# Performance work log

Measured on AMD Instinct MI355X. Metric: run time of the kernel, lower is better.

## Reference

```python
import jax, jax.numpy as jnp
import numpy as np

B, T, D, H = 4096, 200, 128, 128


def setup_inputs() -> dict:
    key = jax.random.key(0)
    ks = jax.random.split(key, 9)
    s = 1.0 / np.sqrt(D + H)  # torch Linear default init bound
    u = lambda k, shape: jax.random.uniform(k, shape, jnp.float32, -s, s)
    return {
        "inputs": jax.random.normal(ks[0], (B, T, D), jnp.float32),
        "attention_scores": jax.random.uniform(ks[1], (B, T), jnp.float32),
        "h0": jnp.zeros((B, H), jnp.float32),
        "Wz": u(ks[2], (D + H, H)), "bz": u(ks[3], (H,)),
        "Wr": u(ks[4], (D + H, H)), "br": u(ks[5], (H,)),
        "Wh": u(ks[6], (D + H, H)), "bh": u(ks[7], (H,)),
    }


def reference(inputs, attention_scores, h0, Wz, bz, Wr, br, Wh, bh):
    # AUGRU: GRU with attention-modulated update gate (DIEN Sec 3.3).
    def step(h, xs):
        x_t, a_t = xs  # [B,D], [B]
        comb = jnp.concatenate([x_t, h], axis=-1)            # [B, D+H]
        z = jax.nn.sigmoid(comb @ Wz + bz)                   # [B, H]
        r = jax.nn.sigmoid(comb @ Wr + br)                   # [B, H]
        comb_r = jnp.concatenate([x_t, r * h], axis=-1)      # [B, D+H]
        h_tilde = jnp.tanh(comb_r @ Wh + bh)                 # [B, H]
        zp = a_t[:, None] * z                                # attention-scaled update gate
        h_new = (1.0 - zp) * h + zp * h_tilde
        return h_new, None

    xs = (jnp.swapaxes(inputs, 0, 1),            # [T, B, D]
          jnp.swapaxes(attention_scores, 0, 1))  # [T, B]
    h_final, _ = jax.lax.scan(step, h0, xs)
    return h_final  # [B, H]
```

## Files before the change

kernel.cpp:

```cpp
#include <hip/hip_runtime.h>
#include <stdint.h>

#define BB 4096
#define TT 200
#define DD 128
#define HH 128

typedef __attribute__((ext_vector_type(8))) short bf16x8;
typedef __attribute__((ext_vector_type(4))) float f32x4;

__device__ __forceinline__ short f2bf(float f) {
    uint32_t u = __builtin_bit_cast(uint32_t, f);
    u += 0x7fffu + ((u >> 16) & 1u);
    return (short)(u >> 16);
}
__device__ __forceinline__ uint32_t pk2(float a, float b) {
    uint32_t r;
    asm("v_cvt_pk_bf16_f32 %0, %1, %2" : "=v"(r) : "v"(a), "v"(b));
    return r;
}
__device__ __forceinline__ float sigm(float x) {
    return __builtin_amdgcn_rcpf(1.0f + __expf(-x));
}
__device__ __forceinline__ float tanhf_(float x) {
    return 2.0f * __builtin_amdgcn_rcpf(1.0f + __expf(-2.0f * x)) - 1.0f;
}
__device__ __forceinline__ void bar_lds() {
    asm volatile("s_waitcnt lgkmcnt(0)" ::: "memory");
    __builtin_amdgcn_sched_barrier(0);
    __builtin_amdgcn_s_barrier();
    __builtin_amdgcn_sched_barrier(0);
}


#define STEP(T, XR) { \
    const int sn_ = ((T) + 1) & 1; \
    *(uint2*)((short*)&xbuf[sn_][xrow][xg_swz] + xhalf) = \
        make_uint2(pk2(XR.x, XR.y), pk2(XR.z, XR.w)); \
    { const int t3_ = ((T) + 3 < TT) ? (T) + 3 : TT - 1; \
      XR = *(const float4*)(xsrc + (size_t)t3_ * DD); } \
    bf16x8 hf_[4]; \
    _Pragma("unroll") \
    for (int kt = 0; kt < 4; ++kt) hf_[kt] = hrow[fg[kt]]; \
    f32x4 az_ = pz, ar_ = pr; \
    _Pragma("unroll") \
    for (int kt = 0; kt < 4; ++kt) { \
        az_ = __builtin_amdgcn_mfma_f32_16x16x32_bf16(Wf[0][1][kt], hf_[kt], az_, 0, 0, 0); \
        ar_ = __builtin_amdgcn_mfma_f32_16x16x32_bf16(Wf[1][1][kt], hf_[kt], ar_, 0, 0, 0); \
    } \
    f32x4 zv_, rhv_; \
    _Pragma("unroll") \
    for (int r = 0; r < 4; ++r) { zv_[r] = sigm(az_[r]); rhv_[r] = sigm(ar_[r]) * hreg[r]; } \
    *(uint2*)((short*)&rhbuf[c][g_out_swz] + ohalf) = \
        make_uint2(pk2(rhv_[0], rhv_[1]), pk2(rhv_[2], rhv_[3])); \
    bar_lds(); \
    const float a_c_ = attbuf[c][(T)]; \
    bf16x8 rf_[4], xf2_[4]; \
    { const bf16x8* xp2_ = &xbuf[sn_][c][0]; \
      _Pragma("unroll") \
      for (int kt = 0; kt < 4; ++kt) { \
          rf_[kt]  = rhrow[fg[kt]]; \
          xf2_[kt] = xp2_[fg[kt]]; \
      } } \
    f32x4 ah_ = ph; \
    _Pragma("unroll") \
    for (int kt = 0; kt < 4; ++kt) \
        ah_ = __builtin_amdgcn_mfma_f32_16x16x32_bf16(Wf[2][1][kt], rf_[kt], ah_, 0, 0, 0); \
    pz = bzv; pr = brv; ph = bhv; \
    _Pragma("unroll") \
    for (int kt = 0; kt < 4; ++kt) { \
        pz = __builtin_amdgcn_mfma_f32_16x16x32_bf16(Wf[0][0][kt], xf2_[kt], pz, 0, 0, 0); \
        pr = __builtin_amdgcn_mfma_f32_16x16x32_bf16(Wf[1][0][kt], xf2_[kt], pr, 0, 0, 0); \
        ph = __builtin_amdgcn_mfma_f32_16x16x32_bf16(Wf[2][0][kt], xf2_[kt], ph, 0, 0, 0); \
    } \
    _Pragma("unroll") \
    for (int r = 0; r < 4; ++r) { \
        float ht_ = tanhf_(ah_[r]); \
        float zp_ = a_c_ * zv_[r]; \
        hreg[r] = __builtin_fmaf(zp_, ht_ - hreg[r], hreg[r]); \
    } \
    *(uint2*)((short*)&hbuf[c][g_out_swz] + ohalf) = \
        make_uint2(pk2(hreg[0], hreg[1]), pk2(hreg[2], hreg[3])); \
    bar_lds(); \
}

__global__ __launch_bounds__(512, 2) void augru_kernel(
    const float* __restrict__ inp,
    const float* __restrict__ att,
    const float* __restrict__ h0,
    const float* __restrict__ Wz, const float* __restrict__ bz,
    const float* __restrict__ Wr, const float* __restrict__ br,
    const float* __restrict__ Wh, const float* __restrict__ bh,
    float* __restrict__ out)
{
    __shared__ bf16x8 xbuf[2][16][16];
    __shared__ bf16x8 hbuf[16][16];
    __shared__ bf16x8 rhbuf[16][16];
    __shared__ float attbuf[16][201];

    const int tid  = threadIdx.x;
    const int wave = tid >> 6;
    const int lane = tid & 63;
    const int c    = lane & 15;
    const int grp  = lane >> 4;
    const int wbase = wave * 16;
    const int ocol  = wbase + grp * 4;
    const int rowbase = blockIdx.x * 16;

    const int swz = c & 7;
    const int fg[4] = { (0 + grp) ^ swz, (4 + grp) ^ swz,
                        (8 + grp) ^ swz, (12 + grp) ^ swz };
    const int g_out_swz = (wave * 2 + (grp >> 1)) ^ swz;
    const int ohalf = (grp & 1) * 4;
    const bf16x8* hrow  = &hbuf[c][0];
    const bf16x8* rhrow = &rhbuf[c][0];

    bf16x8 Wf[3][2][4];
    {
        const float* Wp[3] = {Wz, Wr, Wh};
        #pragma unroll
        for (int g3 = 0; g3 < 3; ++g3) {
            #pragma unroll
            for (int p = 0; p < 2; ++p) {
                #pragma unroll
                for (int kt = 0; kt < 4; ++kt) {
                    bf16x8 v;
                    #pragma unroll
                    for (int j = 0; j < 8; ++j) {
                        int k = p * 128 + kt * 32 + grp * 8 + j;
                        v[j] = f2bf(Wp[g3][(size_t)k * HH + wbase + c]);
                    }
                    Wf[g3][p][kt] = v;
                }
            }
        }
    }
    f32x4 bzv, brv, bhv;
    #pragma unroll
    for (int r = 0; r < 4; ++r) {
        bzv[r] = bz[ocol + r];
        brv[r] = br[ocol + r];
        bhv[r] = bh[ocol + r];
    }

    for (int idx = tid; idx < 16 * TT; idx += 512)
        attbuf[idx / TT][idx % TT] = att[(size_t)rowbase * TT + idx];

    f32x4 hreg;
    {
        float4 hv = *(const float4*)&h0[(size_t)(rowbase + c) * HH + ocol];
        hreg[0] = hv.x; hreg[1] = hv.y; hreg[2] = hv.z; hreg[3] = hv.w;
        *(uint2*)((short*)&hbuf[c][g_out_swz] + ohalf) =
            make_uint2(pk2(hv.x, hv.y), pk2(hv.z, hv.w));
    }

    const int xrow = tid >> 5;
    const int xc4  = (tid & 31) * 4;
    const int xg_swz = ((tid & 31) >> 1) ^ (xrow & 7);
    const int xhalf  = (tid & 1) * 4;
    const float* xsrc = inp + ((size_t)(rowbase + xrow) * TT) * DD + xc4;
    {
        float4 x0 = *(const float4*)(xsrc);
        *(uint2*)((short*)&xbuf[0][xrow][xg_swz] + xhalf) =
            make_uint2(pk2(x0.x, x0.y), pk2(x0.z, x0.w));
    }
    float4 xrA = *(const float4*)(xsrc + DD);
    float4 xrB = *(const float4*)(xsrc + 2 * DD);
    __syncthreads();

    f32x4 pz = bzv, pr = brv, ph = bhv;
    {
        const bf16x8* x0p = &xbuf[0][c][0];
        bf16x8 xf[4];
        #pragma unroll
        for (int kt = 0; kt < 4; ++kt) xf[kt] = x0p[fg[kt]];
        #pragma unroll
        for (int kt = 0; kt < 4; ++kt) {
            pz = __builtin_amdgcn_mfma_f32_16x16x32_bf16(Wf[0][0][kt], xf[kt], pz, 0, 0, 0);
            pr = __builtin_amdgcn_mfma_f32_16x16x32_bf16(Wf[1][0][kt], xf[kt], pr, 0, 0, 0);
            ph = __builtin_amdgcn_mfma_f32_16x16x32_bf16(Wf[2][0][kt], xf[kt], ph, 0, 0, 0);
        }
    }

    for (int t = 0; t < TT; t += 2) {
        STEP(t, xrA);
        STEP(t + 1, xrB);
    }

    float4 o; o.x = hreg[0]; o.y = hreg[1]; o.z = hreg[2]; o.w = hreg[3];
    *(float4*)&out[(size_t)(rowbase + c) * HH + ocol] = o;
}

extern "C" void kernel_launch(void* const* d_in, const int* in_sizes, int n_in,
                              void* d_out, int out_size, void* d_ws, size_t ws_size,
                              hipStream_t stream) {
    const float* inp = (const float*)d_in[0];
    const float* att = (const float*)d_in[1];
    const float* h0  = (const float*)d_in[2];
    const float* Wz  = (const float*)d_in[3];
    const float* bz  = (const float*)d_in[4];
    const float* Wr  = (const float*)d_in[5];
    const float* br  = (const float*)d_in[6];
    const float* Wh  = (const float*)d_in[7];
    const float* bh  = (const float*)d_in[8];
    float* out = (float*)d_out;

    dim3 grid(BB / 16), block(512);
    augru_kernel<<<grid, block, 0, stream>>>(inp, att, h0, Wz, bz, Wr, br, Wh, bh, out);
}
```

Before: 216.4 us.

## Halve waves per block, giving each wave two 16-column output tiles

The block shrinks from 512 to 256 threads, and each wave now computes 32 hidden columns as two 16-column MFMA tiles instead of one. The aim is to cut barrier cost per step, since fewer waves synchronise, and to give each wave more independent MFMA chains to hide latency. The trade-off is double the register-resident weight fragments, since Wf grows to 96 bf16x8 per lane, and launch bounds of 1 block of 256 threads, which lowers occupancy and may cause spills. The x staging also changes to 8 floats per thread with 16-byte LDS stores.

```diff
diff --git a/kernel.cpp b/kernel.cpp
--- a/kernel.cpp
+++ b/kernel.cpp
@@ -33,26 +33,39 @@
 }
 
 
-#define STEP(T, XR) { \
+#define STEP(T, XR0, XR1) { \
     const int sn_ = ((T) + 1) & 1; \
-    *(uint2*)((short*)&xbuf[sn_][xrow][xg_swz] + xhalf) = \
-        make_uint2(pk2(XR.x, XR.y), pk2(XR.z, XR.w)); \
+    *(uint4*)&xbuf[sn_][xrow][xg_swz] = \
+        make_uint4(pk2(XR0.x, XR0.y), pk2(XR0.z, XR0.w), \
+                   pk2(XR1.x, XR1.y), pk2(XR1.z, XR1.w)); \
     { const int t3_ = ((T) + 3 < TT) ? (T) + 3 : TT - 1; \
-      XR = *(const float4*)(xsrc + (size_t)t3_ * DD); } \
+      XR0 = *(const float4*)(xsrc + (size_t)t3_ * DD); \
+      XR1 = *(const float4*)(xsrc + (size_t)t3_ * DD + 4); } \
     bf16x8 hf_[4]; \
     _Pragma("unroll") \
     for (int kt = 0; kt < 4; ++kt) hf_[kt] = hrow[fg[kt]]; \
-    f32x4 az_ = pz, ar_ = pr; \
+    f32x4 az_[2], ar_[2]; \
+    _Pragma("unroll") \
+    for (int ct = 0; ct < 2; ++ct) { az_[ct] = pz[ct]; ar_[ct] = pr[ct]; } \
     _Pragma("unroll") \
     for (int kt = 0; kt < 4; ++kt) { \
-        az_ = __builtin_amdgcn_mfma_f32_16x16x32_bf16(Wf[0][1][kt], hf_[kt], az_, 0, 0, 0); \
-        ar_ = __builtin_amdgcn_mfma_f32_16x16x32_bf16(Wf[1][1][kt], hf_[kt], ar_, 0, 0, 0); \
-    } \
-    f32x4 zv_, rhv_; \
-    _Pragma("unroll") \
-    for (int r = 0; r < 4; ++r) { zv_[r] = sigm(az_[r]); rhv_[r] = sigm(ar_[r]) * hreg[r]; } \
-    *(uint2*)((short*)&rhbuf[c][g_out_swz] + ohalf) = \
-        make_uint2(pk2(rhv_[0], rhv_[1]), pk2(rhv_[2], rhv_[3])); \
+        _Pragma("unroll") \
+        for (int ct = 0; ct < 2; ++ct) { \
+            az_[ct] = __builtin_amdgcn_mfma_f32_16x16x32_bf16(Wf[0][1][kt][ct], hf_[kt], az_[ct], 0, 0, 0); \
+            ar_[ct] = __builtin_amdgcn_mfma_f32_16x16x32_bf16(Wf[1][1][kt][ct], hf_[kt], ar_[ct], 0, 0, 0); \
+        } \
+    } \
+    f32x4 zv_[2], rhv_[2]; \
+    _Pragma("unroll") \
+    for (int ct = 0; ct < 2; ++ct) { \
+        _Pragma("unroll") \
+        for (int r = 0; r < 4; ++r) { \
+            zv_[ct][r]  = sigm(az_[ct][r]); \
+            rhv_[ct][r] = sigm(ar_[ct][r]) * hreg[ct][r]; \
+        } \
+        *(uint2*)((short*)&rhbuf[c][gout[ct]] + ohalf) = \
+            make_uint2(pk2(rhv_[ct][0], rhv_[ct][1]), pk2(rhv_[ct][2], rhv_[ct][3])); \
+    } \
     bar_lds(); \
     const float a_c_ = attbuf[c][(T)]; \
     bf16x8 rf_[4], xf2_[4]; \
@@ -62,29 +75,41 @@
           rf_[kt]  = rhrow[fg[kt]]; \
           xf2_[kt] = xp2_[fg[kt]]; \
       } } \
-    f32x4 ah_ = ph; \
-    _Pragma("unroll") \
-    for (int kt = 0; kt < 4; ++kt) \
-        ah_ = __builtin_amdgcn_mfma_f32_16x16x32_bf16(Wf[2][1][kt], rf_[kt], ah_, 0, 0, 0); \
-    pz = bzv; pr = brv; ph = bhv; \
+    f32x4 ah_[2]; \
+    _Pragma("unroll") \
+    for (int ct = 0; ct < 2; ++ct) ah_[ct] = ph[ct]; \
     _Pragma("unroll") \
     for (int kt = 0; kt < 4; ++kt) { \
-        pz = __builtin_amdgcn_mfma_f32_16x16x32_bf16(Wf[0][0][kt], xf2_[kt], pz, 0, 0, 0); \
-        pr = __builtin_amdgcn_mfma_f32_16x16x32_bf16(Wf[1][0][kt], xf2_[kt], pr, 0, 0, 0); \
-        ph = __builtin_amdgcn_mfma_f32_16x16x32_bf16(Wf[2][0][kt], xf2_[kt], ph, 0, 0, 0); \
-    } \
-    _Pragma("unroll") \
-    for (int r = 0; r < 4; ++r) { \
-        float ht_ = tanhf_(ah_[r]); \
-        float zp_ = a_c_ * zv_[r]; \
-        hreg[r] = __builtin_fmaf(zp_, ht_ - hreg[r], hreg[r]); \
-    } \
-    *(uint2*)((short*)&hbuf[c][g_out_swz] + ohalf) = \
-        make_uint2(pk2(hreg[0], hreg[1]), pk2(hreg[2], hreg[3])); \
+        _Pragma("unroll") \
+        for (int ct = 0; ct < 2; ++ct) \
+            ah_[ct] = __builtin_amdgcn_mfma_f32_16x16x32_bf16(Wf[2][1][kt][ct], rf_[kt], ah_[ct], 0, 0, 0); \
+    } \
+    _Pragma("unroll") \
+    for (int ct = 0; ct < 2; ++ct) { pz[ct] = bzv[ct]; pr[ct] = brv[ct]; ph[ct] = bhv[ct]; } \
+    _Pragma("unroll") \
+    for (int kt = 0; kt < 4; ++kt) { \
+        _Pragma("unroll") \
+        for (int ct = 0; ct < 2; ++ct) { \
+            pz[ct] = __builtin_amdgcn_mfma_f32_16x16x32_bf16(Wf[0][0][kt][ct], xf2_[kt], pz[ct], 0, 0, 0); \
+            pr[ct] = __builtin_amdgcn_mfma_f32_16x16x32_bf16(Wf[1][0][kt][ct], xf2_[kt], pr[ct], 0, 0, 0); \
+            ph[ct] = __builtin_amdgcn_mfma_f32_16x16x32_bf16(Wf[2][0][kt][ct], xf2_[kt], ph[ct], 0, 0, 0); \
+        } \
+    } \
+    _Pragma("unroll") \
+    for (int ct = 0; ct < 2; ++ct) { \
+        _Pragma("unroll") \
+        for (int r = 0; r < 4; ++r) { \
+            float ht_ = tanhf_(ah_[ct][r]); \
+            float zp_ = a_c_ * zv_[ct][r]; \
+            hreg[ct][r] = __builtin_fmaf(zp_, ht_ - hreg[ct][r], hreg[ct][r]); \
+        } \
+        *(uint2*)((short*)&hbuf[c][gout[ct]] + ohalf) = \
+            make_uint2(pk2(hreg[ct][0], hreg[ct][1]), pk2(hreg[ct][2], hreg[ct][3])); \
+    } \
     bar_lds(); \
 }
 
-__global__ __launch_bounds__(512, 2) void augru_kernel(
+__global__ __launch_bounds__(256, 1) void augru_kernel(
     const float* __restrict__ inp,
     const float* __restrict__ att,
     const float* __restrict__ h0,
@@ -103,19 +128,20 @@
     const int lane = tid & 63;
     const int c    = lane & 15;
     const int grp  = lane >> 4;
-    const int wbase = wave * 16;
-    const int ocol  = wbase + grp * 4;
+    const int wbase = wave * 32;
     const int rowbase = blockIdx.x * 16;
 
     const int swz = c & 7;
     const int fg[4] = { (0 + grp) ^ swz, (4 + grp) ^ swz,
                         (8 + grp) ^ swz, (12 + grp) ^ swz };
-    const int g_out_swz = (wave * 2 + (grp >> 1)) ^ swz;
+    const int oc[2]   = { wbase + grp * 4, wbase + 16 + grp * 4 };
+    const int gout[2] = { (4 * wave + (grp >> 1)) ^ swz,
+                          (4 * wave + 2 + (grp >> 1)) ^ swz };
     const int ohalf = (grp & 1) * 4;
     const bf16x8* hrow  = &hbuf[c][0];
     const bf16x8* rhrow = &rhbuf[c][0];
 
-    bf16x8 Wf[3][2][4];
+    bf16x8 Wf[3][2][4][2];
     {
         const float* Wp[3] = {Wz, Wr, Wh};
         #pragma unroll
@@ -124,51 +150,62 @@
             for (int p = 0; p < 2; ++p) {
                 #pragma unroll
                 for (int kt = 0; kt < 4; ++kt) {
-                    bf16x8 v;
                     #pragma unroll
-                    for (int j = 0; j < 8; ++j) {
-                        int k = p * 128 + kt * 32 + grp * 8 + j;
-                        v[j] = f2bf(Wp[g3][(size_t)k * HH + wbase + c]);
+                    for (int ct = 0; ct < 2; ++ct) {
+                        bf16x8 v;
+                        #pragma unroll
+                        for (int j = 0; j < 8; ++j) {
+                            int k = p * 128 + kt * 32 + grp * 8 + j;
+                            v[j] = f2bf(Wp[g3][(size_t)k * HH + wbase + ct * 16 + c]);
+                        }
+                        Wf[g3][p][kt][ct] = v;
                     }
-                    Wf[g3][p][kt] = v;
                 }
             }
         }
     }
-    f32x4 bzv, brv, bhv;
-    #pragma unroll
-    for (int r = 0; r < 4; ++r) {
-        bzv[r] = bz[ocol + r];
-        brv[r] = br[ocol + r];
-        bhv[r] = bh[ocol + r];
-    }
-
-    for (int idx = tid; idx < 16 * TT; idx += 512)
+    f32x4 bzv[2], brv[2], bhv[2];
+    #pragma unroll
+    for (int ct = 0; ct < 2; ++ct)
+        #pragma unroll
+        for (int r = 0; r < 4; ++r) {
+            bzv[ct][r] = bz[oc[ct] + r];
+            brv[ct][r] = br[oc[ct] + r];
+            bhv[ct][r] = bh[oc[ct] + r];
+        }
+
+    for (int idx = tid; idx < 16 * TT; idx += 256)
         attbuf[idx / TT][idx % TT] = att[(size_t)rowbase * TT + idx];
 
-    f32x4 hreg;
+    f32x4 hreg[2];
+    #pragma unroll
+    for (int ct = 0; ct < 2; ++ct) {
+        float4 hv = *(const float4*)&h0[(size_t)(rowbase + c) * HH + oc[ct]];
+        hreg[ct][0] = hv.x; hreg[ct][1] = hv.y; hreg[ct][2] = hv.z; hreg[ct][3] = hv.w;
+        *(uint2*)((short*)&hbuf[c][gout[ct]] + ohalf) =
+            make_uint2(pk2(hv.x, hv.y), pk2(hv.z, hv.w));
+    }
+
+    const int xrow = tid >> 4;
+    const int xc8  = (tid & 15) * 8;
+    const int xg_swz = (tid & 15) ^ (xrow & 7);
+    const float* xsrc = inp + ((size_t)(rowbase + xrow) * TT) * DD + xc8;
     {
-        float4 hv = *(const float4*)&h0[(size_t)(rowbase + c) * HH + ocol];
-        hreg[0] = hv.x; hreg[1] = hv.y; hreg[2] = hv.z; hreg[3] = hv.w;
-        *(uint2*)((short*)&hbuf[c][g_out_swz] + ohalf) =
-            make_uint2(pk2(hv.x, hv.y), pk2(hv.z, hv.w));
-    }
-
-    const int xrow = tid >> 5;
-    const int xc4  = (tid & 31) * 4;
-    const int xg_swz = ((tid & 31) >> 1) ^ (xrow & 7);
-    const int xhalf  = (tid & 1) * 4;
-    const float* xsrc = inp + ((size_t)(rowbase + xrow) * TT) * DD + xc4;
-    {
-        float4 x0 = *(const float4*)(xsrc);
-        *(uint2*)((short*)&xbuf[0][xrow][xg_swz] + xhalf) =
-            make_uint2(pk2(x0.x, x0.y), pk2(x0.z, x0.w));
-    }
-    float4 xrA = *(const float4*)(xsrc + DD);
-    float4 xrB = *(const float4*)(xsrc + 2 * DD);
+        float4 x0a = *(const float4*)(xsrc);
+        float4 x0b = *(const float4*)(xsrc + 4);
+        *(uint4*)&xbuf[0][xrow][xg_swz] =
+            make_uint4(pk2(x0a.x, x0a.y), pk2(x0a.z, x0a.w),
+                       pk2(x0b.x, x0b.y), pk2(x0b.z, x0b.w));
+    }
+    float4 xrA0 = *(const float4*)(xsrc + DD);
+    float4 xrA1 = *(const float4*)(xsrc + DD + 4);
+    float4 xrB0 = *(const float4*)(xsrc + 2 * DD);
+    float4 xrB1 = *(const float4*)(xsrc + 2 * DD + 4);
     __syncthreads();
 
-    f32x4 pz = bzv, pr = brv, ph = bhv;
+    f32x4 pz[2], pr[2], ph[2];
+    #pragma unroll
+    for (int ct = 0; ct < 2; ++ct) { pz[ct] = bzv[ct]; pr[ct] = brv[ct]; ph[ct] = bhv[ct]; }
     {
         const bf16x8* x0p = &xbuf[0][c][0];
         bf16x8 xf[4];
@@ -176,19 +213,25 @@
         for (int kt = 0; kt < 4; ++kt) xf[kt] = x0p[fg[kt]];
         #pragma unroll
         for (int kt = 0; kt < 4; ++kt) {
-            pz = __builtin_amdgcn_mfma_f32_16x16x32_bf16(Wf[0][0][kt], xf[kt], pz, 0, 0, 0);
-            pr = __builtin_amdgcn_mfma_f32_16x16x32_bf16(Wf[1][0][kt], xf[kt], pr, 0, 0, 0);
-            ph = __builtin_amdgcn_mfma_f32_16x16x32_bf16(Wf[2][0][kt], xf[kt], ph, 0, 0, 0);
+            #pragma unroll
+            for (int ct = 0; ct < 2; ++ct) {
+                pz[ct] = __builtin_amdgcn_mfma_f32_16x16x32_bf16(Wf[0][0][kt][ct], xf[kt], pz[ct], 0, 0, 0);
+                pr[ct] = __builtin_amdgcn_mfma_f32_16x16x32_bf16(Wf[1][0][kt][ct], xf[kt], pr[ct], 0, 0, 0);
+                ph[ct] = __builtin_amdgcn_mfma_f32_16x16x32_bf16(Wf[2][0][kt][ct], xf[kt], ph[ct], 0, 0, 0);
+            }
         }
     }
 
     for (int t = 0; t < TT; t += 2) {
-        STEP(t, xrA);
-        STEP(t + 1, xrB);
-    }
-
-    float4 o; o.x = hreg[0]; o.y = hreg[1]; o.z = hreg[2]; o.w = hreg[3];
-    *(float4*)&out[(size_t)(rowbase + c) * HH + ocol] = o;
+        STEP(t, xrA0, xrA1);
+        STEP(t + 1, xrB0, xrB1);
+    }
+
+    #pragma unroll
+    for (int ct = 0; ct < 2; ++ct) {
+        float4 o; o.x = hreg[ct][0]; o.y = hreg[ct][1]; o.z = hreg[ct][2]; o.w = hreg[ct][3];
+        *(float4*)&out[(size_t)(rowbase + c) * HH + oc[ct]] = o;
+    }
 }
 
 extern "C" void kernel_launch(void* const* d_in, const int* in_sizes, int n_in,
@@ -205,6 +248,6 @@
     const float* bh  = (const float*)d_in[8];
     float* out = (float*)d_out;
 
-    dim3 grid(BB / 16), block(512);
+    dim3 grid(BB / 16), block(256);
     augru_kernel<<<grid, block, 0, stream>>>(inp, att, h0, Wz, bz, Wr, br, Wh, bh, out);
 }
```

Measured after the change: 216.8 us. About the same (+0.2%).

## Split waves into input-projection producers and recurrent consumers via LDS double buffer

Applied to the files above, without the earlier changes.

Waves are specialised: four producer waves compute the x-projection for the next timestep (loading x straight from global into registers), and four consumer waves do the h-dependent recurrent MFMAs and gate math. The two groups exchange pre-activations through a double-buffered fp32 LDS array. The aim is to take the input-projection MFMAs off the serial recurrent critical path. In exchange, each consumer wave now covers 32 output columns instead of 16, so per-step recurrent work per wave doubles. LDS use also grows and the occupancy hint of two blocks per SM is dropped.

```diff
diff --git a/kernel.cpp b/kernel.cpp
--- a/kernel.cpp
+++ b/kernel.cpp
@@ -24,6 +24,12 @@
 }
 __device__ __forceinline__ float tanhf_(float x) {
     return 2.0f * __builtin_amdgcn_rcpf(1.0f + __expf(-2.0f * x)) - 1.0f;
+}
+__device__ __forceinline__ bf16x8 mk8(float4 a, float4 b) {
+    union { uint32_t u[4]; bf16x8 v; } q;
+    q.u[0] = pk2(a.x, a.y); q.u[1] = pk2(a.z, a.w);
+    q.u[2] = pk2(b.x, b.y); q.u[3] = pk2(b.z, b.w);
+    return q.v;
 }
 __device__ __forceinline__ void bar_lds() {
     asm volatile("s_waitcnt lgkmcnt(0)" ::: "memory");
@@ -31,60 +37,10 @@
     __builtin_amdgcn_s_barrier();
     __builtin_amdgcn_sched_barrier(0);
 }
-
-
-#define STEP(T, XR) { \
-    const int sn_ = ((T) + 1) & 1; \
-    *(uint2*)((short*)&xbuf[sn_][xrow][xg_swz] + xhalf) = \
-        make_uint2(pk2(XR.x, XR.y), pk2(XR.z, XR.w)); \
-    { const int t3_ = ((T) + 3 < TT) ? (T) + 3 : TT - 1; \
-      XR = *(const float4*)(xsrc + (size_t)t3_ * DD); } \
-    bf16x8 hf_[4]; \
-    _Pragma("unroll") \
-    for (int kt = 0; kt < 4; ++kt) hf_[kt] = hrow[fg[kt]]; \
-    f32x4 az_ = pz, ar_ = pr; \
-    _Pragma("unroll") \
-    for (int kt = 0; kt < 4; ++kt) { \
-        az_ = __builtin_amdgcn_mfma_f32_16x16x32_bf16(Wf[0][1][kt], hf_[kt], az_, 0, 0, 0); \
-        ar_ = __builtin_amdgcn_mfma_f32_16x16x32_bf16(Wf[1][1][kt], hf_[kt], ar_, 0, 0, 0); \
-    } \
-    f32x4 zv_, rhv_; \
-    _Pragma("unroll") \
-    for (int r = 0; r < 4; ++r) { zv_[r] = sigm(az_[r]); rhv_[r] = sigm(ar_[r]) * hreg[r]; } \
-    *(uint2*)((short*)&rhbuf[c][g_out_swz] + ohalf) = \
-        make_uint2(pk2(rhv_[0], rhv_[1]), pk2(rhv_[2], rhv_[3])); \
-    bar_lds(); \
-    const float a_c_ = attbuf[c][(T)]; \
-    bf16x8 rf_[4], xf2_[4]; \
-    { const bf16x8* xp2_ = &xbuf[sn_][c][0]; \
-      _Pragma("unroll") \
-      for (int kt = 0; kt < 4; ++kt) { \
-          rf_[kt]  = rhrow[fg[kt]]; \
-          xf2_[kt] = xp2_[fg[kt]]; \
-      } } \
-    f32x4 ah_ = ph; \
-    _Pragma("unroll") \
-    for (int kt = 0; kt < 4; ++kt) \
-        ah_ = __builtin_amdgcn_mfma_f32_16x16x32_bf16(Wf[2][1][kt], rf_[kt], ah_, 0, 0, 0); \
-    pz = bzv; pr = brv; ph = bhv; \
-    _Pragma("unroll") \
-    for (int kt = 0; kt < 4; ++kt) { \
-        pz = __builtin_amdgcn_mfma_f32_16x16x32_bf16(Wf[0][0][kt], xf2_[kt], pz, 0, 0, 0); \
-        pr = __builtin_amdgcn_mfma_f32_16x16x32_bf16(Wf[1][0][kt], xf2_[kt], pr, 0, 0, 0); \
-        ph = __builtin_amdgcn_mfma_f32_16x16x32_bf16(Wf[2][0][kt], xf2_[kt], ph, 0, 0, 0); \
-    } \
-    _Pragma("unroll") \
-    for (int r = 0; r < 4; ++r) { \
-        float ht_ = tanhf_(ah_[r]); \
-        float zp_ = a_c_ * zv_[r]; \
-        hreg[r] = __builtin_fmaf(zp_, ht_ - hreg[r], hreg[r]); \
-    } \
-    *(uint2*)((short*)&hbuf[c][g_out_swz] + ohalf) = \
-        make_uint2(pk2(hreg[0], hreg[1]), pk2(hreg[2], hreg[3])); \
-    bar_lds(); \
-}
-
-__global__ __launch_bounds__(512, 2) void augru_kernel(
+#define MFMA16 __builtin_amdgcn_mfma_f32_16x16x32_bf16
+
+
+__global__ __launch_bounds__(512) void augru_kernel(
     const float* __restrict__ inp,
     const float* __restrict__ att,
     const float* __restrict__ h0,
@@ -93,102 +49,224 @@
     const float* __restrict__ Wh, const float* __restrict__ bh,
     float* __restrict__ out)
 {
-    __shared__ bf16x8 xbuf[2][16][16];
     __shared__ bf16x8 hbuf[16][16];
     __shared__ bf16x8 rhbuf[16][16];
-    __shared__ float attbuf[16][201];
+    __shared__ float  pff[2][3][16][132];
+    __shared__ float  attbuf[16][201];
+    __shared__ float  biasLDS[3][132];
 
     const int tid  = threadIdx.x;
     const int wave = tid >> 6;
     const int lane = tid & 63;
     const int c    = lane & 15;
     const int grp  = lane >> 4;
-    const int wbase = wave * 16;
-    const int ocol  = wbase + grp * 4;
+    const int wsub = wave & 3;
+    const bool cons = (wave < 4);
+    const int wbase = wsub * 32;
     const int rowbase = blockIdx.x * 16;
 
     const int swz = c & 7;
     const int fg[4] = { (0 + grp) ^ swz, (4 + grp) ^ swz,
                         (8 + grp) ^ swz, (12 + grp) ^ swz };
-    const int g_out_swz = (wave * 2 + (grp >> 1)) ^ swz;
+    const int oc[2]   = { wbase + grp * 4, wbase + 16 + grp * 4 };
+    const int gout[2] = { (4 * wsub + (grp >> 1)) ^ swz,
+                          (4 * wsub + 2 + (grp >> 1)) ^ swz };
     const int ohalf = (grp & 1) * 4;
     const bf16x8* hrow  = &hbuf[c][0];
     const bf16x8* rhrow = &rhbuf[c][0];
 
-    bf16x8 Wf[3][2][4];
+    bf16x8 W[3][4][2];
     {
-        const float* Wp[3] = {Wz, Wr, Wh};
-        #pragma unroll
-        for (int g3 = 0; g3 < 3; ++g3) {
-            #pragma unroll
-            for (int p = 0; p < 2; ++p) {
-                #pragma unroll
-                for (int kt = 0; kt < 4; ++kt) {
+        const float* Wp3[3] = {Wz, Wr, Wh};
+        const int kbase = cons ? 128 : 0;
+        #pragma unroll
+        for (int g3 = 0; g3 < 3; ++g3)
+            #pragma unroll
+            for (int kt = 0; kt < 4; ++kt)
+                #pragma unroll
+                for (int ct = 0; ct < 2; ++ct) {
                     bf16x8 v;
                     #pragma unroll
                     for (int j = 0; j < 8; ++j) {
-                        int k = p * 128 + kt * 32 + grp * 8 + j;
-                        v[j] = f2bf(Wp[g3][(size_t)k * HH + wbase + c]);
+                        int k = kbase + kt * 32 + grp * 8 + j;
+                        v[j] = f2bf(Wp3[g3][(size_t)k * HH + wbase + ct * 16 + c]);
                     }
-                    Wf[g3][p][kt] = v;
-                }
-            }
-        }
-    }
-    f32x4 bzv, brv, bhv;
-    #pragma unroll
-    for (int r = 0; r < 4; ++r) {
-        bzv[r] = bz[ocol + r];
-        brv[r] = br[ocol + r];
-        bhv[r] = bh[ocol + r];
+                    W[g3][kt][ct] = v;
+                }
     }
 
     for (int idx = tid; idx < 16 * TT; idx += 512)
         attbuf[idx / TT][idx % TT] = att[(size_t)rowbase * TT + idx];
-
-    f32x4 hreg;
     {
-        float4 hv = *(const float4*)&h0[(size_t)(rowbase + c) * HH + ocol];
-        hreg[0] = hv.x; hreg[1] = hv.y; hreg[2] = hv.z; hreg[3] = hv.w;
-        *(uint2*)((short*)&hbuf[c][g_out_swz] + ohalf) =
-            make_uint2(pk2(hv.x, hv.y), pk2(hv.z, hv.w));
-    }
-
-    const int xrow = tid >> 5;
-    const int xc4  = (tid & 31) * 4;
-    const int xg_swz = ((tid & 31) >> 1) ^ (xrow & 7);
-    const int xhalf  = (tid & 1) * 4;
-    const float* xsrc = inp + ((size_t)(rowbase + xrow) * TT) * DD + xc4;
-    {
-        float4 x0 = *(const float4*)(xsrc);
-        *(uint2*)((short*)&xbuf[0][xrow][xg_swz] + xhalf) =
-            make_uint2(pk2(x0.x, x0.y), pk2(x0.z, x0.w));
-    }
-    float4 xrA = *(const float4*)(xsrc + DD);
-    float4 xrB = *(const float4*)(xsrc + 2 * DD);
+        const float* Bp3[3] = {bz, br, bh};
+        for (int idx = tid; idx < 3 * 128; idx += 512)
+            biasLDS[idx >> 7][idx & 127] = Bp3[idx >> 7][idx & 127];
+    }
+
+    f32x4 hreg[2];
+    float4 S[8];
+    const float* xsrcP = inp + (size_t)(rowbase + c) * TT * DD + grp * 8;
+
+    if (cons) {
+        #pragma unroll
+        for (int ct = 0; ct < 2; ++ct) {
+            float4 hv = *(const float4*)&h0[(size_t)(rowbase + c) * HH + oc[ct]];
+            hreg[ct][0] = hv.x; hreg[ct][1] = hv.y; hreg[ct][2] = hv.z; hreg[ct][3] = hv.w;
+            *(uint2*)((short*)&hbuf[c][gout[ct]] + ohalf) =
+                make_uint2(pk2(hv.x, hv.y), pk2(hv.z, hv.w));
+        }
+    } else {
+        f32x4 paz[2], par[2], pah[2];
+        #pragma unroll
+        for (int ct = 0; ct < 2; ++ct) {
+            paz[ct] = *(const f32x4*)&bz[oc[ct]];
+            par[ct] = *(const f32x4*)&br[oc[ct]];
+            pah[ct] = *(const f32x4*)&bh[oc[ct]];
+        }
+        bf16x8 xf0[4];
+        #pragma unroll
+        for (int kt = 0; kt < 4; ++kt) {
+            float4 a = *(const float4*)(xsrcP + kt * 32);
+            float4 b = *(const float4*)(xsrcP + kt * 32 + 4);
+            xf0[kt] = mk8(a, b);
+        }
+        #pragma unroll
+        for (int kt = 0; kt < 4; ++kt)
+            #pragma unroll
+            for (int ct = 0; ct < 2; ++ct) {
+                paz[ct] = MFMA16(W[0][kt][ct], xf0[kt], paz[ct], 0, 0, 0);
+                par[ct] = MFMA16(W[1][kt][ct], xf0[kt], par[ct], 0, 0, 0);
+                pah[ct] = MFMA16(W[2][kt][ct], xf0[kt], pah[ct], 0, 0, 0);
+            }
+        #pragma unroll
+        for (int ct = 0; ct < 2; ++ct) {
+            *(f32x4*)&pff[0][0][c][oc[ct]] = paz[ct];
+            *(f32x4*)&pff[0][1][c][oc[ct]] = par[ct];
+            *(f32x4*)&pff[0][2][c][oc[ct]] = pah[ct];
+        }
+        const float* p = xsrcP + DD;
+        #pragma unroll
+        for (int kt = 0; kt < 4; ++kt) {
+            S[2 * kt]     = *(const float4*)(p + kt * 32);
+            S[2 * kt + 1] = *(const float4*)(p + kt * 32 + 4);
+        }
+    }
     __syncthreads();
 
-    f32x4 pz = bzv, pr = brv, ph = bhv;
-    {
-        const bf16x8* x0p = &xbuf[0][c][0];
-        bf16x8 xf[4];
-        #pragma unroll
-        for (int kt = 0; kt < 4; ++kt) xf[kt] = x0p[fg[kt]];
-        #pragma unroll
-        for (int kt = 0; kt < 4; ++kt) {
-            pz = __builtin_amdgcn_mfma_f32_16x16x32_bf16(Wf[0][0][kt], xf[kt], pz, 0, 0, 0);
-            pr = __builtin_amdgcn_mfma_f32_16x16x32_bf16(Wf[1][0][kt], xf[kt], pr, 0, 0, 0);
-            ph = __builtin_amdgcn_mfma_f32_16x16x32_bf16(Wf[2][0][kt], xf[kt], ph, 0, 0, 0);
-        }
-    }
-
-    for (int t = 0; t < TT; t += 2) {
-        STEP(t, xrA);
-        STEP(t + 1, xrB);
-    }
-
-    float4 o; o.x = hreg[0]; o.y = hreg[1]; o.z = hreg[2]; o.w = hreg[3];
-    *(float4*)&out[(size_t)(rowbase + c) * HH + ocol] = o;
+    for (int t = 0; t < TT; ++t) {
+        const int slot = t & 1, nslot = slot ^ 1;
+        bf16x8 xfp[4];
+        f32x4 zsave[2];
+
+        if (cons) {
+            f32x4 az[2], ar[2];
+            #pragma unroll
+            for (int ct = 0; ct < 2; ++ct) {
+                az[ct] = *(const f32x4*)&pff[slot][0][c][oc[ct]];
+                ar[ct] = *(const f32x4*)&pff[slot][1][c][oc[ct]];
+            }
+            bf16x8 hf[4];
+            #pragma unroll
+            for (int kt = 0; kt < 4; ++kt) hf[kt] = hrow[fg[kt]];
+            #pragma unroll
+            for (int kt = 0; kt < 4; ++kt)
+                #pragma unroll
+                for (int ct = 0; ct < 2; ++ct) {
+                    az[ct] = MFMA16(W[0][kt][ct], hf[kt], az[ct], 0, 0, 0);
+                    ar[ct] = MFMA16(W[1][kt][ct], hf[kt], ar[ct], 0, 0, 0);
+                }
+            #pragma unroll
+            for (int ct = 0; ct < 2; ++ct) {
+                f32x4 rhv;
+                #pragma unroll
+                for (int r = 0; r < 4; ++r) {
+                    zsave[ct][r] = sigm(az[ct][r]);
+                    rhv[r]       = sigm(ar[ct][r]) * hreg[ct][r];
+                }
+                *(uint2*)((short*)&rhbuf[c][gout[ct]] + ohalf) =
+                    make_uint2(pk2(rhv[0], rhv[1]), pk2(rhv[2], rhv[3]));
+            }
+        } else {
+            #pragma unroll
+            for (int kt = 0; kt < 4; ++kt) xfp[kt] = mk8(S[2 * kt], S[2 * kt + 1]);
+            {
+                const int tn = (t + 2 < TT) ? t + 2 : TT - 1;
+                const float* p = xsrcP + (size_t)tn * DD;
+                #pragma unroll
+                for (int kt = 0; kt < 4; ++kt) {
+                    S[2 * kt]     = *(const float4*)(p + kt * 32);
+                    S[2 * kt + 1] = *(const float4*)(p + kt * 32 + 4);
+                }
+            }
+            f32x4 paz[2], par[2];
+            #pragma unroll
+            for (int ct = 0; ct < 2; ++ct) {
+                paz[ct] = *(const f32x4*)&biasLDS[0][oc[ct]];
+                par[ct] = *(const f32x4*)&biasLDS[1][oc[ct]];
+            }
+            #pragma unroll
+            for (int kt = 0; kt < 4; ++kt)
+                #pragma unroll
+                for (int ct = 0; ct < 2; ++ct) {
+                    paz[ct] = MFMA16(W[0][kt][ct], xfp[kt], paz[ct], 0, 0, 0);
+                    par[ct] = MFMA16(W[1][kt][ct], xfp[kt], par[ct], 0, 0, 0);
+                }
+            #pragma unroll
+            for (int ct = 0; ct < 2; ++ct) {
+                *(f32x4*)&pff[nslot][0][c][oc[ct]] = paz[ct];
+                *(f32x4*)&pff[nslot][1][c][oc[ct]] = par[ct];
+            }
+        }
+        bar_lds();
+        if (cons) {
+            f32x4 ah[2];
+            #pragma unroll
+            for (int ct = 0; ct < 2; ++ct)
+                ah[ct] = *(const f32x4*)&pff[slot][2][c][oc[ct]];
+            bf16x8 rf[4];
+            #pragma unroll
+            for (int kt = 0; kt < 4; ++kt) rf[kt] = rhrow[fg[kt]];
+            #pragma unroll
+            for (int kt = 0; kt < 4; ++kt)
+                #pragma unroll
+                for (int ct = 0; ct < 2; ++ct)
+                    ah[ct] = MFMA16(W[2][kt][ct], rf[kt], ah[ct], 0, 0, 0);
+            const float a_c = attbuf[c][t];
+            #pragma unroll
+            for (int ct = 0; ct < 2; ++ct) {
+                #pragma unroll
+                for (int r = 0; r < 4; ++r) {
+                    float ht = tanhf_(ah[ct][r]);
+                    float zp = a_c * zsave[ct][r];
+                    hreg[ct][r] = __builtin_fmaf(zp, ht - hreg[ct][r], hreg[ct][r]);
+                }
+                *(uint2*)((short*)&hbuf[c][gout[ct]] + ohalf) =
+                    make_uint2(pk2(hreg[ct][0], hreg[ct][1]), pk2(hreg[ct][2], hreg[ct][3]));
+            }
+        } else {
+            f32x4 pah[2];
+            #pragma unroll
+            for (int ct = 0; ct < 2; ++ct)
+                pah[ct] = *(const f32x4*)&biasLDS[2][oc[ct]];
+            #pragma unroll
+            for (int kt = 0; kt < 4; ++kt)
+                #pragma unroll
+                for (int ct = 0; ct < 2; ++ct)
+                    pah[ct] = MFMA16(W[2][kt][ct], xfp[kt], pah[ct], 0, 0, 0);
+            #pragma unroll
+            for (int ct = 0; ct < 2; ++ct)
+                *(f32x4*)&pff[nslot][2][c][oc[ct]] = pah[ct];
+        }
+        bar_lds();
+    }
+
+    if (cons) {
+        #pragma unroll
+        for (int ct = 0; ct < 2; ++ct) {
+            float4 o; o.x = hreg[ct][0]; o.y = hreg[ct][1]; o.z = hreg[ct][2]; o.w = hreg[ct][3];
+            *(float4*)&out[(size_t)(rowbase + c) * HH + oc[ct]] = o;
+        }
+    }
 }
 
 extern "C" void kernel_launch(void* const* d_in, const int* in_sizes, int n_in,
```

Result: slower. 278.0 us (+28.5%).
